# Kernel optimization log

Hardware: AMD Instinct MI355X
Metric: run time of the kernel (lower is better)

The kernel has to match this reference:

```python
import jax, jax.numpy as jnp
import numpy as np

N_MOV, N_CREW, N_CAST = 200000, 100000, 100000
E = 600000
H, OUT = 128, 16


def _sage(x_src, x_dst, src, dst, Wl, Wr, b, n_dst):
    # PyG SAGEConv: lin_l(mean_{j in N(i)} x_src[j]) + lin_r(x_dst[i]); bias lives in lin_l
    msg = jax.ops.segment_sum(x_src[src], dst, num_segments=n_dst)
    cnt = jax.ops.segment_sum(jnp.ones(src.shape, x_src.dtype), dst, num_segments=n_dst)
    agg = msg / jnp.maximum(cnt, 1.0)[:, None]
    return agg @ Wl + b + x_dst @ Wr


def setup_inputs() -> dict:
    key = jax.random.key(0)
    kit = iter(jax.random.split(key, 64))
    def rn(shape, s=0.05):
        return jax.random.normal(next(kit), shape, jnp.float32) * s
    inp = {
        'x_movies': rn((N_MOV, 128), 1.0),
        'x_crew': rn((N_CREW, 64), 1.0),
        'x_cast': rn((N_CAST, 64), 1.0),
        'src_cm': jax.random.randint(next(kit), (E,), 0, N_CREW),
        'dst_cm': jax.random.randint(next(kit), (E,), 0, N_MOV),
        'src_am': jax.random.randint(next(kit), (E,), 0, N_CAST),
        'dst_am': jax.random.randint(next(kit), (E,), 0, N_MOV),
    }
    # (src_dim, dst_dim) per relation at layer 0; layer 1 uses H for both
    dims = {'cm': (64, 128), 'am': (64, 128), 'mc': (128, 64), 'ma': (128, 64)}
    for l in range(2):
        for rel, (ds, dd) in dims.items():
            if l > 0:
                ds, dd = H, H
            inp[f'Wl_{rel}_{l}'] = rn((ds, H))
            inp[f'Wr_{rel}_{l}'] = rn((dd, H))
            inp[f'b_{rel}_{l}'] = jnp.zeros((H,), jnp.float32)
    inp['lin_W'] = rn((H, OUT))
    inp['lin_b'] = jnp.zeros((OUT,), jnp.float32)
    return inp


def reference(x_movies, x_crew, x_cast, src_cm, dst_cm, src_am, dst_am,
              Wl_cm_0, Wr_cm_0, b_cm_0, Wl_am_0, Wr_am_0, b_am_0,
              Wl_mc_0, Wr_mc_0, b_mc_0, Wl_ma_0, Wr_ma_0, b_ma_0,
              Wl_cm_1, Wr_cm_1, b_cm_1, Wl_am_1, Wr_am_1, b_am_1,
              Wl_mc_1, Wr_mc_1, b_mc_1, Wl_ma_1, Wr_ma_1, b_ma_1,
              lin_W, lin_b):
    params = [
        {'cm': (Wl_cm_0, Wr_cm_0, b_cm_0), 'am': (Wl_am_0, Wr_am_0, b_am_0),
         'mc': (Wl_mc_0, Wr_mc_0, b_mc_0), 'ma': (Wl_ma_0, Wr_ma_0, b_ma_0)},
        {'cm': (Wl_cm_1, Wr_cm_1, b_cm_1), 'am': (Wl_am_1, Wr_am_1, b_am_1),
         'mc': (Wl_mc_1, Wr_mc_1, b_mc_1), 'ma': (Wl_ma_1, Wr_ma_1, b_ma_1)},
    ]
    xm, xc, xa = x_movies, x_crew, x_cast
    for p in params:  # dropout is identity in eval mode
        # movies receives from crew and cast; HeteroConv aggr='mean' over the 2 relations
        m = 0.5 * (_sage(xc, xm, src_cm, dst_cm, *p['cm'], N_MOV)
                   + _sage(xa, xm, src_am, dst_am, *p['am'], N_MOV))
        # reverse relations: movies -> crew / cast (flip edge direction)
        c = _sage(xm, xc, dst_cm, src_cm, *p['mc'], N_CREW)
        a = _sage(xm, xa, dst_am, src_am, *p['ma'], N_CAST)
        xm, xc, xa = jax.nn.relu(m), jax.nn.relu(c), jax.nn.relu(a)
    return xm @ lin_W + lin_b
```

## Files before the change

kernel.cpp:

```cpp
#include <hip/hip_runtime.h>

#define TPB 256
typedef unsigned int uint;
typedef unsigned short ushort;
typedef long long ll;
typedef __attribute__((ext_vector_type(8))) short bf16x8;
typedef __attribute__((ext_vector_type(8))) ushort u16x8;
typedef __attribute__((ext_vector_type(4))) float f32x4;

__device__ __forceinline__ float bf2f(ushort h) {
  return __uint_as_float(((uint)h) << 16);
}
__device__ __forceinline__ ushort f2bf(float f) {
  uint u = __float_as_uint(f);
  u += 0x7fffu + ((u >> 16) & 1u);
  return (ushort)(u >> 16);
}

struct PJobs {
  const float* a[10];
  const float* bavg[10];
  ushort* out[10];
  const float* ba[2];
  const float* bb[2];
  float* bo[2];
};

__global__ __launch_bounds__(TPB) void mega1_k(
    const float* __restrict__ xm, ushort* __restrict__ xmh, ll n8, int gConv,
    const int* __restrict__ src_cm, const int* __restrict__ dst_cm,
    const int* __restrict__ src_am, const int* __restrict__ dst_am, int E, int g2E,
    int* __restrict__ cnt_m_cm, int* __restrict__ cnt_m_am,
    int* __restrict__ cnt_c, int* __restrict__ cnt_a,
    int* __restrict__ rk_m_cm, int* __restrict__ rk_c,
    int* __restrict__ rk_m_am, int* __restrict__ rk_a,
    PJobs J) {
  int b = blockIdx.x;
  int t = threadIdx.x;
  if (b < gConv) {
    ll i = (ll)b * TPB + t;
    if (i >= n8) return;
    const float* p = xm + i * 8;
    float4 a = *(const float4*)p;
    float4 bb = *(const float4*)(p + 4);
    u16x8 v;
    v[0] = f2bf(a.x); v[1] = f2bf(a.y); v[2] = f2bf(a.z); v[3] = f2bf(a.w);
    v[4] = f2bf(bb.x); v[5] = f2bf(bb.y); v[6] = f2bf(bb.z); v[7] = f2bf(bb.w);
    *(u16x8*)&xmh[i * 8] = v;
    return;
  }
  b -= gConv;
  if (b < g2E) {
    int i = b * TPB + t;
    if (i < E) {
      rk_m_cm[i] = atomicAdd(&cnt_m_cm[dst_cm[i]], 1);
      rk_c[i]    = atomicAdd(&cnt_c[src_cm[i]], 1);
    } else if (i < 2 * E) {
      int e = i - E;
      rk_m_am[e] = atomicAdd(&cnt_m_am[dst_am[e]], 1);
      rk_a[e]    = atomicAdd(&cnt_a[src_am[e]], 1);
    }
    return;
  }
  b -= g2E;
  if (b == 512) {
    if (t < 128) J.bo[0][t] = 0.5f * (J.ba[0][t] + J.bb[0][t]);
    else if (t < 256) J.bo[1][t - 128] = 0.5f * (J.ba[1][t - 128] + J.bb[1][t - 128]);
    return;
  }
  int job, idx, K;
  if (b < 384) { job = b >> 6; idx = ((b & 63) << 8) | t; K = 128; }
  else { int bb2 = b - 384; job = 6 + (bb2 >> 5); idx = ((bb2 & 31) << 8) | t; K = 64; }
  int col = idx / K, k = idx - col * K;
  float v = J.a[job][k * 128 + col];
  if (J.bavg[job]) v = 0.5f * (v + J.bavg[job][k * 128 + col]);
  J.out[job][idx] = f2bf(v);
}

__device__ __forceinline__ void rel_map(int b, int nb0, int nb1, int nb2, int nb3,
                                        int& r, int& lb) {
  if (b < nb0) { r = 0; lb = b; }
  else if (b < nb0 + nb1) { r = 1; lb = b - nb0; }
  else if (b < nb0 + nb1 + nb2) { r = 2; lb = b - nb0 - nb1; }
  else { r = 3; lb = b - nb0 - nb1 - nb2; }
}

__global__ __launch_bounds__(TPB) void bsum_rinv_k(
    const int* __restrict__ c0, int n0, const int* __restrict__ c1, int n1,
    const int* __restrict__ c2, int n2, const int* __restrict__ c3, int n3,
    int* __restrict__ bsum, float* __restrict__ rinv, int nm2, int total, int nbtot) {
  __shared__ int lds[TPB];
  int b = blockIdx.x;
  int t = threadIdx.x;
  if (b >= nbtot) {
    int i = (b - nbtot) * TPB + t;
    if (i < total) {
      float scale = (i < nm2) ? 0.5f : 1.0f;
      rinv[i] = scale / fmaxf((float)c0[i], 1.0f);
    }
    return;
  }
  int nb0 = (n0 + TPB - 1) / TPB, nb1 = (n1 + TPB - 1) / TPB;
  int nb2 = (n2 + TPB - 1) / TPB, nb3 = (n3 + TPB - 1) / TPB;
  int r, lb;
  rel_map(b, nb0, nb1, nb2, nb3, r, lb);
  const int* cnt = (r == 0) ? c0 : (r == 1) ? c1 : (r == 2) ? c2 : c3;
  int n = (r == 0) ? n0 : (r == 1) ? n1 : (r == 2) ? n2 : n3;
  int i = lb * TPB + t;
  lds[t] = (i < n) ? cnt[i] : 0;
  __syncthreads();
  for (int off = 128; off > 0; off >>= 1) {
    if (t < off) lds[t] += lds[t + off];
    __syncthreads();
  }
  if (t == 0) bsum[r * 1024 + lb] = lds[0];
}

__global__ __launch_bounds__(TPB) void scan_all_k(int* __restrict__ bsum,
                                                  int n0, int n1, int n2, int n3) {
  __shared__ int lds[TPB];
  int r = blockIdx.x;
  int n = (r == 0) ? n0 : (r == 1) ? n1 : (r == 2) ? n2 : n3;
  int nb = (n + TPB - 1) / TPB;
  int* bs = bsum + r * 1024;
  int t = threadIdx.x;
  int offset = 0;
  for (int base = 0; base < nb; base += TPB) {
    int v = (base + t < nb) ? bs[base + t] : 0;
    lds[t] = v;
    __syncthreads();
    for (int off = 1; off < TPB; off <<= 1) {
      int add = (t >= off) ? lds[t - off] : 0;
      __syncthreads();
      lds[t] += add;
      __syncthreads();
    }
    int incl = lds[t];
    if (base + t < nb) bs[base + t] = offset + incl - v;
    int tot = lds[TPB - 1];
    __syncthreads();
    offset += tot;
  }
}

__global__ __launch_bounds__(TPB) void finalize_all_k(
    const int* __restrict__ c0, int n0, int* __restrict__ rp0,
    const int* __restrict__ c1, int n1, int* __restrict__ rp1,
    const int* __restrict__ c2, int n2, int* __restrict__ rp2,
    const int* __restrict__ c3, int n3, int* __restrict__ rp3,
    const int* __restrict__ bsum) {
  __shared__ int lds[TPB];
  int nb0 = (n0 + TPB - 1) / TPB, nb1 = (n1 + TPB - 1) / TPB;
  int nb2 = (n2 + TPB - 1) / TPB, nb3 = (n3 + TPB - 1) / TPB;
  int r, lb;
  rel_map(blockIdx.x, nb0, nb1, nb2, nb3, r, lb);
  const int* cnt = (r == 0) ? c0 : (r == 1) ? c1 : (r == 2) ? c2 : c3;
  int* rowptr = (r == 0) ? rp0 : (r == 1) ? rp1 : (r == 2) ? rp2 : rp3;
  int n = (r == 0) ? n0 : (r == 1) ? n1 : (r == 2) ? n2 : n3;
  int t = threadIdx.x;
  int i = lb * TPB + t;
  int v = (i < n) ? cnt[i] : 0;
  lds[t] = v;
  __syncthreads();
  for (int off = 1; off < TPB; off <<= 1) {
    int add = (t >= off) ? lds[t - off] : 0;
    __syncthreads();
    lds[t] += add;
    __syncthreads();
  }
  int ex = lds[t] - v + bsum[r * 1024 + lb];
  if (i < n) {
    rowptr[i] = ex;
    if (i == n - 1) rowptr[n] = ex + v;
  }
}

__global__ __launch_bounds__(TPB) void fillr_k(const int* __restrict__ src_cm,
                                               const int* __restrict__ dst_cm,
                                               const int* __restrict__ src_am,
                                               const int* __restrict__ dst_am, int E,
                                               const int* __restrict__ rp_m_cm,
                                               const int* __restrict__ rp_m_am,
                                               const int* __restrict__ rp_c,
                                               const int* __restrict__ rp_a,
                                               const int* __restrict__ rk_m_cm,
                                               const int* __restrict__ rk_c,
                                               const int* __restrict__ rk_m_am,
                                               const int* __restrict__ rk_a,
                                               int* __restrict__ pm_m_cm,
                                               int* __restrict__ pm_m_am,
                                               int* __restrict__ pm_c,
                                               int* __restrict__ pm_a) {
  int i = blockIdx.x * blockDim.x + threadIdx.x;
  if (i < E) {
    int s = src_cm[i], d = dst_cm[i];
    pm_m_cm[rp_m_cm[d] + rk_m_cm[i]] = s;
    pm_c[rp_c[s] + rk_c[i]] = d;
  } else if (i < 2 * E) {
    int e = i - E;
    int s = src_am[e], d = dst_am[e];
    pm_m_am[rp_m_am[d] + rk_m_am[e]] = s;
    pm_a[rp_a[s] + rk_a[e]] = d;
  }
}

__global__ __launch_bounds__(TPB) void gatherw2_k(
    const ushort* __restrict__ xmh,
    const int* __restrict__ rp1, const int* __restrict__ pm1,
    const float* __restrict__ ri1, int N1, ushort* __restrict__ o1,
    const int* __restrict__ rp2, const int* __restrict__ pm2,
    const float* __restrict__ ri2, int N2, ushort* __restrict__ o2, int g1) {
  int b = blockIdx.x;
  const int* rowptr; const int* perm; const float* rinv; int N; ushort* out;
  int lb;
  if (b < g1) { rowptr = rp1; perm = pm1; rinv = ri1; N = N1; out = o1; lb = b; }
  else { rowptr = rp2; perm = pm2; rinv = ri2; N = N2; out = o2; lb = b - g1; }
  int nid = lb * 16 + (threadIdx.x >> 4);
  if (nid >= N) return;
  int d = (threadIdx.x & 15) << 3;
  int j = rowptr[nid], e = rowptr[nid + 1];
  float aA[8] = {0.f}, aB[8] = {0.f};
  for (; j + 1 < e; j += 2) {
    u16x8 v0 = *(const u16x8*)&xmh[((ll)perm[j] << 7) + d];
    u16x8 v1 = *(const u16x8*)&xmh[((ll)perm[j + 1] << 7) + d];
#pragma unroll
    for (int k = 0; k < 8; ++k) { aA[k] += bf2f(v0[k]); aB[k] += bf2f(v1[k]); }
  }
  if (j < e) {
    u16x8 v0 = *(const u16x8*)&xmh[((ll)perm[j] << 7) + d];
#pragma unroll
    for (int k = 0; k < 8; ++k) aA[k] += bf2f(v0[k]);
  }
  float r = rinv[nid];
  u16x8 o;
#pragma unroll
  for (int k = 0; k < 8; ++k) o[k] = f2bf((aA[k] + aB[k]) * r);
  *(u16x8*)&out[((ll)nid << 7) + d] = o;
}

__global__ __launch_bounds__(TPB) void gather2_k(
    const ushort* __restrict__ s1, const ushort* __restrict__ s2,
    const int* __restrict__ rp1, const int* __restrict__ pm1, const float* __restrict__ ri1,
    const int* __restrict__ rp2, const int* __restrict__ pm2, const float* __restrict__ ri2,
    int N, ushort* __restrict__ out) {
  int nid = blockIdx.x * 16 + (threadIdx.x >> 4);
  if (nid >= N) return;
  int d = (threadIdx.x & 15) << 3;
  float aA[8] = {0.f}, aB[8] = {0.f};
  {
    int j = rp1[nid], e = rp1[nid + 1];
    for (; j + 1 < e; j += 2) {
      u16x8 v0 = *(const u16x8*)&s1[((ll)pm1[j] << 7) + d];
      u16x8 v1 = *(const u16x8*)&s1[((ll)pm1[j + 1] << 7) + d];
#pragma unroll
      for (int k = 0; k < 8; ++k) { aA[k] += bf2f(v0[k]); aB[k] += bf2f(v1[k]); }
    }
    if (j < e) {
      u16x8 v0 = *(const u16x8*)&s1[((ll)pm1[j] << 7) + d];
#pragma unroll
      for (int k = 0; k < 8; ++k) aA[k] += bf2f(v0[k]);
    }
  }
  float r1 = ri1[nid];
  float res[8];
#pragma unroll
  for (int k = 0; k < 8; ++k) res[k] = (aA[k] + aB[k]) * r1;
  float bA[8] = {0.f}, bB[8] = {0.f};
  {
    int j = rp2[nid], e = rp2[nid + 1];
    for (; j + 1 < e; j += 2) {
      u16x8 v0 = *(const u16x8*)&s2[((ll)pm2[j] << 7) + d];
      u16x8 v1 = *(const u16x8*)&s2[((ll)pm2[j + 1] << 7) + d];
#pragma unroll
      for (int k = 0; k < 8; ++k) { bA[k] += bf2f(v0[k]); bB[k] += bf2f(v1[k]); }
    }
    if (j < e) {
      u16x8 v0 = *(const u16x8*)&s2[((ll)pm2[j] << 7) + d];
#pragma unroll
      for (int k = 0; k < 8; ++k) bA[k] += bf2f(v0[k]);
    }
  }
  float r2 = ri2[nid];
  ushort* p = &out[((ll)nid << 7) + d];
  u16x8 cur = *(u16x8*)p;
  u16x8 o;
#pragma unroll
  for (int k = 0; k < 8; ++k)
    o[k] = f2bf(bf2f(cur[k]) + res[k] + (bA[k] + bB[k]) * r2);
  *(u16x8*)p = o;
}

__global__ __launch_bounds__(TPB) void final_k(const ushort* __restrict__ X,
                                               const float* __restrict__ W,
                                               const float* __restrict__ b,
                                               float* __restrict__ out, int M) {
  __shared__ float lw[128 * 16];
  __shared__ float lb[16];
  int t = threadIdx.x;
  for (int i = t; i < 2048; i += TPB) lw[i] = W[i];
  if (t < 16) lb[t] = b[t];
  __syncthreads();
  ll row = (ll)blockIdx.x * TPB + t;
  if (row >= M) return;
  float acc[16];
#pragma unroll
  for (int c = 0; c < 16; ++c) acc[c] = lb[c];
  const ushort* xr = &X[row * 128];
  for (int k = 0; k < 128; k += 8) {
    u16x8 xv = *(const u16x8*)&xr[k];
#pragma unroll
    for (int j = 0; j < 8; ++j) {
      float xs = fmaxf(bf2f(xv[j]), 0.f);
#pragma unroll
      for (int c = 0; c < 16; ++c) acc[c] = fmaf(xs, lw[(k + j) * 16 + c], acc[c]);
    }
  }
#pragma unroll
  for (int c = 0; c < 16; c += 4) {
    float4 o; o.x = acc[c]; o.y = acc[c + 1]; o.z = acc[c + 2]; o.w = acc[c + 3];
    *(float4*)&out[row * 16 + c] = o;
  }
}

#define BK 64
#define XPITCH 72
#define CPITCH 132
struct CArgs {
  const void* X0; const ushort* WT0; int K0; int xb0;
  const void* X1; const ushort* WT1; int K1; int xb1;
  int nseg; const float* bias; void* out; int M; int nblk;
};

template <bool XRELU>
__global__ __launch_bounds__(TPB) void mfma5_k(CArgs a0, CArgs a1, CArgs a2,
                                               CArgs a3, CArgs a4) {
  const int bx = blockIdx.x;
  const int o0 = a0.nblk, o1 = o0 + a1.nblk, o2 = o1 + a2.nblk, o3 = o2 + a3.nblk;
  const CArgs& a = (bx < o0) ? a0 : (bx < o1) ? a1 : (bx < o2) ? a2
                   : (bx < o3) ? a3 : a4;
  const int blk = bx - ((bx < o0) ? 0 : (bx < o1) ? o0 : (bx < o2) ? o1
                        : (bx < o3) ? o2 : o3);

  __shared__ ushort sbuf[2 * 128 * XPITCH];
  ushort* Xs = sbuf;
  ushort* Ws = sbuf + 128 * XPITCH;
  const int t = threadIdx.x;
  const int lane = t & 63;
  const int wid = t >> 6;
  const int wm = (wid >> 1) << 6;
  const int wn = (wid & 1) << 6;
  const ll rbase = (ll)blk * 128;
  const int M = a.M;

  f32x4 acc[4][4];
#pragma unroll
  for (int mi = 0; mi < 4; ++mi)
#pragma unroll
    for (int ni = 0; ni < 4; ++ni) acc[mi][ni] = (f32x4){0.f, 0.f, 0.f, 0.f};

  for (int s = 0; s < a.nseg; ++s) {
    const void* Xv = s ? a.X1 : a.X0;
    const ushort* WT = s ? a.WT1 : a.WT0;
    const int K = s ? a.K1 : a.K0;
    const int xb = s ? a.xb1 : a.xb0;
    for (int k0 = 0; k0 < K; k0 += BK) {
      __syncthreads();
#pragma unroll
      for (int i = 0; i < 4; ++i) {
        int idx8 = t + i * TPB;
        int row = idx8 >> 3;
        int kb = (idx8 & 7) << 3;
        u16x8 xv;
        ll grow = rbase + row;
        if (grow < M) {
          if (xb) {
            xv = *(const u16x8*)((const ushort*)Xv + grow * K + k0 + kb);
            if (XRELU) {
#pragma unroll
              for (int j = 0; j < 8; ++j) xv[j] = (xv[j] & 0x8000u) ? (ushort)0 : xv[j];
            }
          } else {
            const float* xp = (const float*)Xv + grow * K + k0 + kb;
            float4 va = *(const float4*)xp;
            float4 vb = *(const float4*)(xp + 4);
            if (XRELU) {
              va.x = fmaxf(va.x, 0.f); va.y = fmaxf(va.y, 0.f);
              va.z = fmaxf(va.z, 0.f); va.w = fmaxf(va.w, 0.f);
              vb.x = fmaxf(vb.x, 0.f); vb.y = fmaxf(vb.y, 0.f);
              vb.z = fmaxf(vb.z, 0.f); vb.w = fmaxf(vb.w, 0.f);
            }
            xv[0] = f2bf(va.x); xv[1] = f2bf(va.y); xv[2] = f2bf(va.z); xv[3] = f2bf(va.w);
            xv[4] = f2bf(vb.x); xv[5] = f2bf(vb.y); xv[6] = f2bf(vb.z); xv[7] = f2bf(vb.w);
          }
        } else {
#pragma unroll
          for (int j = 0; j < 8; ++j) xv[j] = 0;
        }
        *(u16x8*)&Xs[row * XPITCH + kb] = xv;
        *(u16x8*)&Ws[row * XPITCH + kb] = *(const u16x8*)(WT + (ll)row * K + k0 + kb);
      }
      __syncthreads();
#pragma unroll
      for (int kk = 0; kk < BK; kk += 32) {
        const int krow = kk + ((lane >> 4) << 3);
        bf16x8 af[4], bfr[4];
#pragma unroll
        for (int mi = 0; mi < 4; ++mi)
          af[mi] = *(const bf16x8*)&Xs[(wm + mi * 16 + (lane & 15)) * XPITCH + krow];
#pragma unroll
        for (int ni = 0; ni < 4; ++ni)
          bfr[ni] = *(const bf16x8*)&Ws[(wn + ni * 16 + (lane & 15)) * XPITCH + krow];
#pragma unroll
        for (int mi = 0; mi < 4; ++mi)
#pragma unroll
          for (int ni = 0; ni < 4; ++ni)
            acc[mi][ni] = __builtin_amdgcn_mfma_f32_16x16x32_bf16(af[mi], bfr[ni],
                                                                  acc[mi][ni], 0, 0, 0);
      }
    }
  }

  __syncthreads();

  {
    const int colb = wn + (lane & 15);
    const int rsub = (lane >> 4) << 2;
#pragma unroll
    for (int ni = 0; ni < 4; ++ni) {
      int col = colb + ni * 16;
      float bv = a.bias ? a.bias[col] : 0.f;
#pragma unroll
      for (int mi = 0; mi < 4; ++mi) {
        int row0 = wm + mi * 16 + rsub;
#pragma unroll
        for (int j = 0; j < 4; ++j)
          sbuf[(row0 + j) * CPITCH + col] = f2bf(acc[mi][ni][j] + bv);
      }
    }
  }
  __syncthreads();
  {
    int lrow = t >> 1;
    int half = t & 1;
    ll grow = rbase + lrow;
    if (grow < M) {
      const ushort* src = &sbuf[lrow * CPITCH + half * 64];
      ushort* dst = (ushort*)a.out + grow * 128 + half * 64;
#pragma unroll
      for (int k = 0; k < 8; ++k)
        *(u16x8*)(dst + k * 8) = *(const u16x8*)(src + k * 8);
    }
  }
}

extern "C" void kernel_launch(void* const* d_in, const int* in_sizes, int n_in,
                              void* d_out, int out_size, void* d_ws, size_t ws_size,
                              hipStream_t stream) {
  const float* xm = (const float*)d_in[0];
  const float* xc = (const float*)d_in[1];
  const float* xa = (const float*)d_in[2];
  const int* src_cm = (const int*)d_in[3];
  const int* dst_cm = (const int*)d_in[4];
  const int* src_am = (const int*)d_in[5];
  const int* dst_am = (const int*)d_in[6];
  const float* Wl_cm_0 = (const float*)d_in[7];
  const float* Wr_cm_0 = (const float*)d_in[8];
  const float* b_cm_0  = (const float*)d_in[9];
  const float* Wl_am_0 = (const float*)d_in[10];
  const float* Wr_am_0 = (const float*)d_in[11];
  const float* b_am_0  = (const float*)d_in[12];
  const float* Wl_mc_0 = (const float*)d_in[13];
  const float* Wr_mc_0 = (const float*)d_in[14];
  const float* b_mc_0  = (const float*)d_in[15];
  const float* Wl_ma_0 = (const float*)d_in[16];
  const float* Wr_ma_0 = (const float*)d_in[17];
  const float* b_ma_0  = (const float*)d_in[18];
  const float* Wl_cm_1 = (const float*)d_in[19];
  const float* Wr_cm_1 = (const float*)d_in[20];
  const float* b_cm_1  = (const float*)d_in[21];
  const float* Wl_am_1 = (const float*)d_in[22];
  const float* Wr_am_1 = (const float*)d_in[23];
  const float* b_am_1  = (const float*)d_in[24];
  const float* lin_W   = (const float*)d_in[31];
  const float* lin_b   = (const float*)d_in[32];

  const int NM = in_sizes[0] / 128;
  const int NC = in_sizes[1] / 64;
  const int NA = in_sizes[2] / 64;
  const int E  = in_sizes[3];
  const int SMAX = (NC > NA) ? NC : NA;

  float* base = (float*)d_ws;
  size_t o = 0;
  ushort* A = (ushort*)(base + o); o += (size_t)NM * 64;
  ushort* xmh = (ushort*)(base + o); o += (size_t)NM * 64;
  float* S = base + o; o += (size_t)SMAX * 128;
  ushort* S3h = (ushort*)(base + o); o += (size_t)SMAX * 64;
  ushort* S4h = (ushort*)(base + o); o += (size_t)SMAX * 64;
  ushort* B = (ushort*)(base + o); o += (size_t)NC * 64;
  ushort* C = (ushort*)(base + o); o += (size_t)NA * 64;
  int* cnt_m_cm = (int*)(base + o); o += NM;
  int* cnt_m_am = (int*)(base + o); o += NM;
  int* cnt_c    = (int*)(base + o); o += NC;
  int* cnt_a    = (int*)(base + o); o += NA;
  float* rinv_m_cm = base + o; o += NM;
  float* rinv_m_am = base + o; o += NM;
  float* rinv_c    = base + o; o += NC;
  float* rinv_a    = base + o; o += NA;
  int* rp_m_cm = (int*)(base + o); o += NM + 1;
  int* rp_m_am = (int*)(base + o); o += NM + 1;
  int* rp_c    = (int*)(base + o); o += NC + 1;
  int* rp_a    = (int*)(base + o); o += NA + 1;
  int* pm_m_cm = (int*)(base + o); o += E;
  int* pm_m_am = (int*)(base + o); o += E;
  int* pm_c    = (int*)(base + o); o += E;
  int* pm_a    = (int*)(base + o); o += E;
  int* bsum    = (int*)(base + o); o += 4096;
  float* b0c  = base + o; o += 128;
  float* b1c  = base + o; o += 128;
  ushort* WT_r0   = (ushort*)(base + o); o += 8192;
  ushort* WT_r1   = (ushort*)(base + o); o += 8192;
  ushort* WT_mc0l = (ushort*)(base + o); o += 8192;
  ushort* WT_ma0l = (ushort*)(base + o); o += 8192;
  ushort* WT_cm1  = (ushort*)(base + o); o += 8192;
  ushort* WT_am1  = (ushort*)(base + o); o += 8192;
  ushort* WT_mc0r = (ushort*)(base + o); o += 4096;
  ushort* WT_ma0r = (ushort*)(base + o); o += 4096;
  ushort* WT_cm0  = (ushort*)(base + o); o += 4096;
  ushort* WT_am0  = (ushort*)(base + o); o += 4096;

  if (ws_size < o * sizeof(float)) return;

  int* rk_m_cm = (int*)S;
  int* rk_c    = rk_m_cm + E;
  int* rk_m_am = rk_m_cm + 2 * E;
  int* rk_a    = rk_m_cm + 3 * E;
  ushort* S1h = (ushort*)S;
  ushort* S2h = S1h + (size_t)SMAX * 128;

  float* outf = (float*)d_out;
  const int g2E = (2 * E + TPB - 1) / TPB;
  const int nbm = (NM + TPB - 1) / TPB;
  const int nbc = (NC + TPB - 1) / TPB;
  const int nba = (NA + TPB - 1) / TPB;
  const int nbtot = 2 * nbm + nbc + nba;
  const int nodes_total = 2 * NM + NC + NA;
  const ll n8 = (ll)NM * 16;
  const int gConv = (int)((n8 + TPB - 1) / TPB);

  PJobs J;
  J.a[0] = Wr_cm_0; J.bavg[0] = Wr_am_0; J.out[0] = WT_r0;
  J.a[1] = Wr_cm_1; J.bavg[1] = Wr_am_1; J.out[1] = WT_r1;
  J.a[2] = Wl_mc_0; J.bavg[2] = nullptr; J.out[2] = WT_mc0l;
  J.a[3] = Wl_ma_0; J.bavg[3] = nullptr; J.out[3] = WT_ma0l;
  J.a[4] = Wl_cm_1; J.bavg[4] = nullptr; J.out[4] = WT_cm1;
  J.a[5] = Wl_am_1; J.bavg[5] = nullptr; J.out[5] = WT_am1;
  J.a[6] = Wr_mc_0; J.bavg[6] = nullptr; J.out[6] = WT_mc0r;
  J.a[7] = Wr_ma_0; J.bavg[7] = nullptr; J.out[7] = WT_ma0r;
  J.a[8] = Wl_cm_0; J.bavg[8] = nullptr; J.out[8] = WT_cm0;
  J.a[9] = Wl_am_0; J.bavg[9] = nullptr; J.out[9] = WT_am0;
  J.ba[0] = b_cm_0; J.bb[0] = b_am_0; J.bo[0] = b0c;
  J.ba[1] = b_cm_1; J.bb[1] = b_am_1; J.bo[1] = b1c;

  hipMemsetAsync(cnt_m_cm, 0, sizeof(int) * (size_t)nodes_total, stream);
  mega1_k<<<gConv + g2E + 513, TPB, 0, stream>>>(
      xm, xmh, n8, gConv, src_cm, dst_cm, src_am, dst_am, E, g2E,
      cnt_m_cm, cnt_m_am, cnt_c, cnt_a, rk_m_cm, rk_c, rk_m_am, rk_a, J);

  {
    int gR = (nodes_total + TPB - 1) / TPB;
    bsum_rinv_k<<<nbtot + gR, TPB, 0, stream>>>(cnt_m_cm, NM, cnt_m_am, NM,
                                                cnt_c, NC, cnt_a, NA, bsum,
                                                rinv_m_cm, 2 * NM, nodes_total, nbtot);
  }
  scan_all_k<<<4, TPB, 0, stream>>>(bsum, NM, NM, NC, NA);
  finalize_all_k<<<nbtot, TPB, 0, stream>>>(cnt_m_cm, NM, rp_m_cm, cnt_m_am, NM, rp_m_am,
                                            cnt_c, NC, rp_c, cnt_a, NA, rp_a, bsum);
  fillr_k<<<g2E, TPB, 0, stream>>>(src_cm, dst_cm, src_am, dst_am, E,
                                   rp_m_cm, rp_m_am, rp_c, rp_a,
                                   rk_m_cm, rk_c, rk_m_am, rk_a,
                                   pm_m_cm, pm_m_am, pm_c, pm_a);

  const int gM = (NM + 127) / 128;
  const int gC = (NC + 127) / 128;
  const int gA = (NA + 127) / 128;
  const int gnM = (NM + 15) / 16;
  const int gwc = (NC + 15) / 16;
  const int gwa = (NA + 15) / 16;
  CArgs Z = {};

  gatherw2_k<<<gwc + gwa, TPB, 0, stream>>>(xmh, rp_c, pm_c, rinv_c, NC, S1h,
                                            rp_a, pm_a, rinv_a, NA, S2h, gwc);
  {
    CArgs ac = {S1h, WT_mc0l, 128, 1, xc, WT_mc0r, 64, 0, 2, b_mc_0, B, NC, gC};
    CArgs aa = {S2h, WT_ma0l, 128, 1, xa, WT_ma0r, 64, 0, 2, b_ma_0, C, NA, gA};
    CArgs am = {xmh, WT_r0, 128, 1, nullptr, nullptr, 0, 0, 1, b0c, A, NM, gM};
    CArgs tc = {xc, WT_cm0, 64, 0, nullptr, nullptr, 0, 0, 1, nullptr, S3h, NC, gC};
    CArgs ta = {xa, WT_am0, 64, 0, nullptr, nullptr, 0, 0, 1, nullptr, S4h, NA, gA};
    mfma5_k<false><<<gC + gA + gM + gC + gA, TPB, 0, stream>>>(ac, aa, am, tc, ta);
  }
  gather2_k<<<gnM, TPB, 0, stream>>>(S3h, S4h, rp_m_cm, pm_m_cm, rinv_m_cm,
                                     rp_m_am, pm_m_am, rinv_m_am, NM, A);

  {
    CArgs am = {A, WT_r1, 128, 1, nullptr, nullptr, 0, 0, 1, b1c, A, NM, gM};
    CArgs ac = {B, WT_cm1, 128, 1, nullptr, nullptr, 0, 0, 1, nullptr, S3h, NC, gC};
    CArgs aa = {C, WT_am1, 128, 1, nullptr, nullptr, 0, 0, 1, nullptr, S4h, NA, gA};
    mfma5_k<true><<<gM + gC + gA, TPB, 0, stream>>>(am, ac, aa, Z, Z);
  }
  gather2_k<<<gnM, TPB, 0, stream>>>(S3h, S4h, rp_m_cm, pm_m_cm, rinv_m_cm,
                                     rp_m_am, pm_m_am, rinv_m_am, NM, A);

  final_k<<<(NM + TPB - 1) / TPB, TPB, 0, stream>>>(A, lin_W, lin_b, outf, NM);
}
```

Baseline: 559.1 us.

## Fuse CSR fill into first GEMM launch and reorder layer-0 schedule

The separate CSR permutation-fill kernel is folded into a combined launch with the layer-0 GEMMs that do not depend on the reverse-relation gathers (movie root, crew/cast transforms). The gather for crew/cast and their two-segment GEMMs now run afterwards in a separate launch. Nontemporal loads and stores are also used for the fp32-to-bf16 conversion of movie features. The goal is to remove one launch and overlap the scatter-heavy fill with MFMA work. The cost is an extra launch for the split GEMM group and a larger kernel that declares its LDS buffer even for fill blocks.

```diff
diff --git a/kernel.cpp b/kernel.cpp
--- a/kernel.cpp
+++ b/kernel.cpp
@@ -40,13 +40,13 @@
   if (b < gConv) {
     ll i = (ll)b * TPB + t;
     if (i >= n8) return;
-    const float* p = xm + i * 8;
-    float4 a = *(const float4*)p;
-    float4 bb = *(const float4*)(p + 4);
+    const f32x4* p = (const f32x4*)(xm + i * 8);
+    f32x4 a = __builtin_nontemporal_load(p);
+    f32x4 bb = __builtin_nontemporal_load(p + 1);
     u16x8 v;
-    v[0] = f2bf(a.x); v[1] = f2bf(a.y); v[2] = f2bf(a.z); v[3] = f2bf(a.w);
-    v[4] = f2bf(bb.x); v[5] = f2bf(bb.y); v[6] = f2bf(bb.z); v[7] = f2bf(bb.w);
-    *(u16x8*)&xmh[i * 8] = v;
+    v[0] = f2bf(a[0]); v[1] = f2bf(a[1]); v[2] = f2bf(a[2]); v[3] = f2bf(a[3]);
+    v[4] = f2bf(bb[0]); v[5] = f2bf(bb[1]); v[6] = f2bf(bb[2]); v[7] = f2bf(bb[3]);
+    __builtin_nontemporal_store(v, (u16x8*)&xmh[i * 8]);
     return;
   }
   b -= gConv;
@@ -175,35 +175,6 @@
   }
 }
 
-__global__ __launch_bounds__(TPB) void fillr_k(const int* __restrict__ src_cm,
-                                               const int* __restrict__ dst_cm,
-                                               const int* __restrict__ src_am,
-                                               const int* __restrict__ dst_am, int E,
-                                               const int* __restrict__ rp_m_cm,
-                                               const int* __restrict__ rp_m_am,
-                                               const int* __restrict__ rp_c,
-                                               const int* __restrict__ rp_a,
-                                               const int* __restrict__ rk_m_cm,
-                                               const int* __restrict__ rk_c,
-                                               const int* __restrict__ rk_m_am,
-                                               const int* __restrict__ rk_a,
-                                               int* __restrict__ pm_m_cm,
-                                               int* __restrict__ pm_m_am,
-                                               int* __restrict__ pm_c,
-                                               int* __restrict__ pm_a) {
-  int i = blockIdx.x * blockDim.x + threadIdx.x;
-  if (i < E) {
-    int s = src_cm[i], d = dst_cm[i];
-    pm_m_cm[rp_m_cm[d] + rk_m_cm[i]] = s;
-    pm_c[rp_c[s] + rk_c[i]] = d;
-  } else if (i < 2 * E) {
-    int e = i - E;
-    int s = src_am[e], d = dst_am[e];
-    pm_m_am[rp_m_am[d] + rk_m_am[e]] = s;
-    pm_a[rp_a[s] + rk_a[e]] = d;
-  }
-}
-
 __global__ __launch_bounds__(TPB) void gatherw2_k(
     const ushort* __restrict__ xmh,
     const int* __restrict__ rp1, const int* __restrict__ pm1,
@@ -330,18 +301,40 @@
   const void* X1; const ushort* WT1; int K1; int xb1;
   int nseg; const float* bias; void* out; int M; int nblk;
 };
+struct FArgs {
+  const int* src_cm; const int* dst_cm; const int* src_am; const int* dst_am; int E;
+  const int* rp_m_cm; const int* rp_m_am; const int* rp_c; const int* rp_a;
+  const int* rk_m_cm; const int* rk_c; const int* rk_m_am; const int* rk_a;
+  int* pm_m_cm; int* pm_m_am; int* pm_c; int* pm_a;
+};
 
 template <bool XRELU>
-__global__ __launch_bounds__(TPB) void mfma5_k(CArgs a0, CArgs a1, CArgs a2,
+__global__ __launch_bounds__(TPB) void mega2_k(FArgs F, int gFill,
+                                               CArgs a0, CArgs a1, CArgs a2,
                                                CArgs a3, CArgs a4) {
-  const int bx = blockIdx.x;
+  __shared__ ushort sbuf[2 * 128 * XPITCH];
+  int bx = blockIdx.x;
+  if (bx < gFill) {
+    int i = bx * TPB + threadIdx.x;
+    if (i < F.E) {
+      int s = F.src_cm[i], d = F.dst_cm[i];
+      F.pm_m_cm[F.rp_m_cm[d] + F.rk_m_cm[i]] = s;
+      F.pm_c[F.rp_c[s] + F.rk_c[i]] = d;
+    } else if (i < 2 * F.E) {
+      int e = i - F.E;
+      int s = F.src_am[e], d = F.dst_am[e];
+      F.pm_m_am[F.rp_m_am[d] + F.rk_m_am[e]] = s;
+      F.pm_a[F.rp_a[s] + F.rk_a[e]] = d;
+    }
+    return;
+  }
+  bx -= gFill;
   const int o0 = a0.nblk, o1 = o0 + a1.nblk, o2 = o1 + a2.nblk, o3 = o2 + a3.nblk;
   const CArgs& a = (bx < o0) ? a0 : (bx < o1) ? a1 : (bx < o2) ? a2
                    : (bx < o3) ? a3 : a4;
   const int blk = bx - ((bx < o0) ? 0 : (bx < o1) ? o0 : (bx < o2) ? o1
                         : (bx < o3) ? o2 : o3);
 
-  __shared__ ushort sbuf[2 * 128 * XPITCH];
   ushort* Xs = sbuf;
   ushort* Ws = sbuf + 128 * XPITCH;
   const int t = threadIdx.x;
@@ -576,10 +569,6 @@
   scan_all_k<<<4, TPB, 0, stream>>>(bsum, NM, NM, NC, NA);
   finalize_all_k<<<nbtot, TPB, 0, stream>>>(cnt_m_cm, NM, rp_m_cm, cnt_m_am, NM, rp_m_am,
                                             cnt_c, NC, rp_c, cnt_a, NA, rp_a, bsum);
-  fillr_k<<<g2E, TPB, 0, stream>>>(src_cm, dst_cm, src_am, dst_am, E,
-                                   rp_m_cm, rp_m_am, rp_c, rp_a,
-                                   rk_m_cm, rk_c, rk_m_am, rk_a,
-                                   pm_m_cm, pm_m_am, pm_c, pm_a);
 
   const int gM = (NM + 127) / 128;
   const int gC = (NC + 127) / 128;
@@ -588,16 +577,25 @@
   const int gwc = (NC + 15) / 16;
   const int gwa = (NA + 15) / 16;
   CArgs Z = {};
-
-  gatherw2_k<<<gwc + gwa, TPB, 0, stream>>>(xmh, rp_c, pm_c, rinv_c, NC, S1h,
-                                            rp_a, pm_a, rinv_a, NA, S2h, gwc);
-  {
-    CArgs ac = {S1h, WT_mc0l, 128, 1, xc, WT_mc0r, 64, 0, 2, b_mc_0, B, NC, gC};
-    CArgs aa = {S2h, WT_ma0l, 128, 1, xa, WT_ma0r, 64, 0, 2, b_ma_0, C, NA, gA};
+  FArgs F = {src_cm, dst_cm, src_am, dst_am, E,
+             rp_m_cm, rp_m_am, rp_c, rp_a,
+             rk_m_cm, rk_c, rk_m_am, rk_a,
+             pm_m_cm, pm_m_am, pm_c, pm_a};
+  FArgs F0 = {};
+
+  {
     CArgs am = {xmh, WT_r0, 128, 1, nullptr, nullptr, 0, 0, 1, b0c, A, NM, gM};
     CArgs tc = {xc, WT_cm0, 64, 0, nullptr, nullptr, 0, 0, 1, nullptr, S3h, NC, gC};
     CArgs ta = {xa, WT_am0, 64, 0, nullptr, nullptr, 0, 0, 1, nullptr, S4h, NA, gA};
-    mfma5_k<false><<<gC + gA + gM + gC + gA, TPB, 0, stream>>>(ac, aa, am, tc, ta);
+    mega2_k<false><<<g2E + gM + gC + gA, TPB, 0, stream>>>(F, g2E, am, tc, ta, Z, Z);
+  }
+
+  gatherw2_k<<<gwc + gwa, TPB, 0, stream>>>(xmh, rp_c, pm_c, rinv_c, NC, S1h,
+                                            rp_a, pm_a, rinv_a, NA, S2h, gwc);
+  {
+    CArgs ac = {S1h, WT_mc0l, 128, 1, xc, WT_mc0r, 64, 0, 2, b_mc_0, B, NC, gC};
+    CArgs aa = {S2h, WT_ma0l, 128, 1, xa, WT_ma0r, 64, 0, 2, b_ma_0, C, NA, gA};
+    mega2_k<false><<<gC + gA, TPB, 0, stream>>>(F0, 0, ac, aa, Z, Z, Z);
   }
   gather2_k<<<gnM, TPB, 0, stream>>>(S3h, S4h, rp_m_cm, pm_m_cm, rinv_m_cm,
                                      rp_m_am, pm_m_am, rinv_m_am, NM, A);
@@ -606,7 +604,7 @@
     CArgs am = {A, WT_r1, 128, 1, nullptr, nullptr, 0, 0, 1, b1c, A, NM, gM};
     CArgs ac = {B, WT_cm1, 128, 1, nullptr, nullptr, 0, 0, 1, nullptr, S3h, NC, gC};
     CArgs aa = {C, WT_am1, 128, 1, nullptr, nullptr, 0, 0, 1, nullptr, S4h, NA, gA};
-    mfma5_k<true><<<gM + gC + gA, TPB, 0, stream>>>(am, ac, aa, Z, Z);
+    mega2_k<true><<<gM + gC + gA, TPB, 0, stream>>>(F0, 0, am, ac, aa, Z, Z);
   }
   gather2_k<<<gnM, TPB, 0, stream>>>(S3h, S4h, rp_m_cm, pm_m_cm, rinv_m_cm,
                                      rp_m_am, pm_m_am, rinv_m_am, NM, A);
```

Measured after the change: 575.9 us. 3.0% more time.
